# Optimization experiments

Hardware: AMD Instinct MI355X
Metric: run time of the kernel (lower is better)

Reference implementation:

```python
import jax, jax.numpy as jnp
import numpy as np

N, IN_DIM, HID, E_DIM, E = 50000, 128, 256, 32, 400000
BN_INV = np.float32(1.0 / np.sqrt(1.0 + 1e-5))  # running_mean=0, running_var=1


def _lin_init(key, fan_in, fan_out):
    kw, kb = jax.random.split(key)
    s = 1.0 / np.sqrt(fan_in)
    W = jax.random.uniform(kw, (fan_in, fan_out), jnp.float32, -s, s)
    b = jax.random.uniform(kb, (fan_out,), jnp.float32, -s, s)
    return W, b


def setup_inputs() -> dict:
    key = jax.random.key(0)
    ks = jax.random.split(key, 12)
    x = jax.random.normal(ks[0], (N, IN_DIM), jnp.float32)
    edge_index = jax.random.randint(ks[1], (2, E), 0, N, jnp.int64)
    edge_attr = jax.random.normal(ks[2], (E, E_DIM), jnp.float32)
    Wn, bn_b = _lin_init(ks[3], IN_DIM, HID)
    We, be = _lin_init(ks[4], E_DIM, HID)
    Wa1, ba1 = _lin_init(ks[5], 2 * HID, HID)
    Wa2, ba2 = _lin_init(ks[6], HID, 1)
    W1, b1 = _lin_init(ks[7], HID, 2 * HID)
    W2, b2 = _lin_init(ks[8], 2 * HID, HID)
    gn = jnp.ones((HID,), jnp.float32); betan = jnp.zeros((HID,), jnp.float32)
    ge = jnp.ones((HID,), jnp.float32); betae = jnp.zeros((HID,), jnp.float32)
    gm = jnp.ones((2 * HID,), jnp.float32); betam = jnp.zeros((2 * HID,), jnp.float32)
    eps = jnp.zeros((1,), jnp.float32)
    return dict(x=x, edge_index=edge_index, edge_attr=edge_attr,
                Wn=Wn, bn_b=bn_b, gn=gn, betan=betan,
                We=We, be=be, ge=ge, betae=betae,
                Wa1=Wa1, ba1=ba1, Wa2=Wa2, ba2=ba2,
                W1=W1, b1=b1, gm=gm, betam=betam, W2=W2, b2=b2, eps=eps)


def _bn(h, g, b):
    # eval-mode BatchNorm1d with running_mean=0, running_var=1
    return h * (g * BN_INV) + b


def reference(x, edge_index, edge_attr, Wn, bn_b, gn, betan, We, be, ge, betae,
              Wa1, ba1, Wa2, ba2, W1, b1, gm, betam, W2, b2, eps):
    h = jax.nn.relu(_bn(x @ Wn + bn_b, gn, betan))           # [N, HID] node_encoder
    ef = jax.nn.relu(_bn(edge_attr @ We + be, ge, betae))    # [E, HID] edge_encoder
    row, col = edge_index[0], edge_index[1]
    ni = h[row]                                              # [E, HID]
    nj = h[col]                                              # [E, HID]
    att_in = jnp.concatenate([ni + ef, nj], axis=-1)         # [E, 2*HID]
    a = jnp.tanh(att_in @ Wa1 + ba1) @ Wa2 + ba2             # [E, 1]
    a = jax.nn.leaky_relu(a, 0.2)
    a = jax.nn.softmax(a, axis=0)                            # softmax over all edges
    msg = (nj + ef) * a                                      # [E, HID]
    agg = jnp.zeros_like(h).at[row].add(msg)                 # scatter-add
    out = (1.0 + eps) * h + agg
    mid = jax.nn.relu(_bn(out @ W1 + b1, gm, betam))         # MLP hidden [N, 2*HID]
    return mid @ W2 + b2                                     # [N, HID]
```

## Files before the change

kernel.cpp:

```cpp
#include <hip/hip_runtime.h>

typedef __attribute__((ext_vector_type(8))) short    s16x8;
typedef __attribute__((ext_vector_type(8))) unsigned short u16x8;
typedef __attribute__((ext_vector_type(4))) unsigned short u16x4;
typedef __attribute__((ext_vector_type(4))) float    f32x4;

#define BN_INV 0.9999950000374997f
#define MAXDEG 64
#define INV64  0.015625f

__device__ __forceinline__ unsigned short f2b(float f) {
    union { float f; unsigned u; } v; v.f = f;
    return (unsigned short)((v.u + 0x7FFFu + ((v.u >> 16) & 1u)) >> 16);
}
__device__ __forceinline__ float b2f(unsigned short b) {
    union { unsigned u; float f; } v; v.u = (unsigned)b << 16;
    return v.f;
}
__device__ __forceinline__ float fast_tanh(float x) {
    float e = __expf(-2.f * fabsf(x));
    float t = (1.f - e) / (1.f + e);
    return copysignf(t, x);
}

__global__ __launch_bounds__(256) void gemm_mfma(
    const void* __restrict__ Av, int lda, int a_f32,
    const unsigned short* __restrict__ BT, int ldb, int bsplit,
    float* __restrict__ Cf, unsigned short* __restrict__ Cb, int ldc,
    const float* __restrict__ bias, const float* __restrict__ gamma,
    const float* __restrict__ beta, int M, int K, int bnrelu)
{
    __shared__ unsigned short As[128 * 40];
    __shared__ unsigned short Bs[128 * 40];

    const int tid = threadIdx.x;
    const int row0 = blockIdx.y * 128;
    const int col0 = blockIdx.x * 128;
    const int w = tid >> 6, l = tid & 63;
    const int wr = (w >> 1) * 64;
    const int wc = (w & 1) * 64;
    const int srow = tid >> 1;
    const int shalf = (tid & 1) * 16;

    f32x4 acc[4][4];
    #pragma unroll
    for (int i = 0; i < 4; ++i)
        #pragma unroll
        for (int j = 0; j < 4; ++j)
            acc[i][j] = (f32x4){0.f, 0.f, 0.f, 0.f};

    const bool arow_ok = (row0 + srow) < M;
    const unsigned short* Ab = (const unsigned short*)Av + (size_t)(row0 + srow) * lda + shalf;
    const float*          Af = (const float*)Av          + (size_t)(row0 + srow) * lda + shalf;
    int bcol = col0 + srow, koff = 0;
    if (bsplit && col0 >= bsplit) { bcol -= bsplit; koff = bsplit; }
    const unsigned short* Bp = BT + (size_t)bcol * ldb + koff + shalf;

    const int lrow = (l >> 4) * 4;
    const int lcol = l & 15;
    const int kfrag = (l >> 4) * 8;

    for (int kt = 0; kt < K; kt += 32) {
        u16x8 av0 = {0, 0, 0, 0, 0, 0, 0, 0};
        u16x8 av1 = {0, 0, 0, 0, 0, 0, 0, 0};
        if (arow_ok) {
            if (a_f32) {
                float4 u0 = *(const float4*)(Af + kt);
                float4 u1 = *(const float4*)(Af + kt + 4);
                float4 u2 = *(const float4*)(Af + kt + 8);
                float4 u3 = *(const float4*)(Af + kt + 12);
                av0 = (u16x8){ f2b(u0.x), f2b(u0.y), f2b(u0.z), f2b(u0.w),
                               f2b(u1.x), f2b(u1.y), f2b(u1.z), f2b(u1.w) };
                av1 = (u16x8){ f2b(u2.x), f2b(u2.y), f2b(u2.z), f2b(u2.w),
                               f2b(u3.x), f2b(u3.y), f2b(u3.z), f2b(u3.w) };
            } else {
                av0 = *(const u16x8*)(Ab + kt);
                av1 = *(const u16x8*)(Ab + kt + 8);
            }
        }
        u16x8 bv0 = *(const u16x8*)(Bp + kt);
        u16x8 bv1 = *(const u16x8*)(Bp + kt + 8);
        *(u16x8*)&As[srow * 40 + shalf]     = av0;
        *(u16x8*)&As[srow * 40 + shalf + 8] = av1;
        *(u16x8*)&Bs[srow * 40 + shalf]     = bv0;
        *(u16x8*)&Bs[srow * 40 + shalf + 8] = bv1;
        __syncthreads();
        s16x8 af[4], bfr[4];
        #pragma unroll
        for (int i = 0; i < 4; ++i)
            af[i] = *(const s16x8*)&As[(wr + i * 16 + lcol) * 40 + kfrag];
        #pragma unroll
        for (int j = 0; j < 4; ++j)
            bfr[j] = *(const s16x8*)&Bs[(wc + j * 16 + lcol) * 40 + kfrag];
        #pragma unroll
        for (int i = 0; i < 4; ++i)
            #pragma unroll
            for (int j = 0; j < 4; ++j)
                acc[i][j] = __builtin_amdgcn_mfma_f32_16x16x32_bf16(
                    af[i], bfr[j], acc[i][j], 0, 0, 0);
        __syncthreads();
    }

    #pragma unroll
    for (int j = 0; j < 4; ++j) {
        const int col = col0 + wc + j * 16 + lcol;
        const float bi = bias ? bias[col] : 0.f;
        float g = 1.f, bt = 0.f;
        if (bnrelu) { g = gamma[col] * BN_INV; bt = beta[col]; }
        #pragma unroll
        for (int i = 0; i < 4; ++i) {
            const int r0 = row0 + wr + i * 16 + lrow;
            #pragma unroll
            for (int q = 0; q < 4; ++q) {
                const int rr = r0 + q;
                if (rr < M) {
                    float v = acc[i][j][q] + bi;
                    if (bnrelu) v = fmaxf(v * g + bt, 0.f);
                    if (Cf) Cf[(size_t)rr * ldc + col] = v;
                    if (Cb) Cb[(size_t)rr * ldc + col] = f2b(v);
                }
            }
        }
    }
}

__global__ __launch_bounds__(512) void fused_edge(
    const float* __restrict__ ea,
    const int* __restrict__ ei,
    const unsigned short* __restrict__ WeT,
    const unsigned char* __restrict__ Wa1T8,
    const unsigned short* __restrict__ HAB,
    const float* __restrict__ be, const float* __restrict__ ge,
    const float* __restrict__ betae, const float* __restrict__ ba1,
    const float* __restrict__ Wa2, const float* __restrict__ ba2,
    unsigned char* __restrict__ EF,
    float* __restrict__ es, float* __restrict__ Ssum, int E)
{
    __shared__ __align__(16) unsigned char smem[32768];
    unsigned short* As  = (unsigned short*)smem;
    unsigned char*  EFs = smem;
    int*   sIdx = (int*)smem;
    float* sRed = (float*)(smem + 1024);

    const int tid = threadIdx.x;
    const int row0 = blockIdx.x * 128;
    const int w = tid >> 6, l = tid & 63;
    const int lgrp = l >> 4, lcol = l & 15;
    const int kfrag = lgrp * 8;

    {
        const int sr = tid >> 2, sk = (tid & 3) * 8;
        u16x8 av = {0, 0, 0, 0, 0, 0, 0, 0};
        if (row0 + sr < E) {
            const float* ap = ea + (size_t)(row0 + sr) * 32 + sk;
            float4 u0 = *(const float4*)ap, u1 = *(const float4*)(ap + 4);
            av = (u16x8){ f2b(u0.x), f2b(u0.y), f2b(u0.z), f2b(u0.w),
                          f2b(u1.x), f2b(u1.y), f2b(u1.z), f2b(u1.w) };
        }
        *(u16x8*)&As[sr * 40 + sk] = av;
    }
    __syncthreads();

    f32x4 acc[4][4];
    #pragma unroll
    for (int i = 0; i < 4; ++i)
        #pragma unroll
        for (int j = 0; j < 4; ++j)
            acc[i][j] = (f32x4){0.f, 0.f, 0.f, 0.f};

    const int wchan = (w & 3) * 64;
    const int wedge = (w >> 2) * 64;
    {
        s16x8 af[4], bfr[4];
        #pragma unroll
        for (int i = 0; i < 4; ++i)
            af[i] = *(const s16x8*)&WeT[(wchan + i * 16 + lcol) * 32 + kfrag];
        #pragma unroll
        for (int j = 0; j < 4; ++j)
            bfr[j] = *(const s16x8*)&As[(wedge + j * 16 + lcol) * 40 + kfrag];
        #pragma unroll
        for (int i = 0; i < 4; ++i)
            #pragma unroll
            for (int j = 0; j < 4; ++j)
                acc[i][j] = __builtin_amdgcn_mfma_f32_16x16x32_bf16(
                    af[i], bfr[j], acc[i][j], 0, 0, 0);
    }
    __syncthreads();

    #pragma unroll
    for (int i = 0; i < 4; ++i) {
        const int ch0 = wchan + i * 16 + lgrp * 4;
        float4 g4 = *(const float4*)(ge + ch0);
        float4 t4 = *(const float4*)(betae + ch0);
        float4 b4 = *(const float4*)(be + ch0);
        g4.x *= BN_INV; g4.y *= BN_INV; g4.z *= BN_INV; g4.w *= BN_INV;
        #pragma unroll
        for (int j = 0; j < 4; ++j) {
            const int edge = wedge + j * 16 + lcol;
            float v0 = fmaxf((acc[i][j][0] + b4.x) * g4.x + t4.x, 0.f);
            float v1 = fmaxf((acc[i][j][1] + b4.y) * g4.y + t4.y, 0.f);
            float v2 = fmaxf((acc[i][j][2] + b4.z) * g4.z + t4.z, 0.f);
            float v3 = fmaxf((acc[i][j][3] + b4.w) * g4.w + t4.w, 0.f);
            int pk = __builtin_amdgcn_cvt_pk_fp8_f32(v0, v1, 0, false);
            pk = __builtin_amdgcn_cvt_pk_fp8_f32(v2, v3, pk, true);
            *(unsigned*)&EFs[edge * 256 + ((((ch0 >> 3) ^ (edge & 7)) << 3) | (ch0 & 7))]
                = (unsigned)pk;
            acc[i][j] = (f32x4){0.f, 0.f, 0.f, 0.f};
        }
    }
    __syncthreads();

    const int wr = (w >> 2) * 64;
    const int wc = (w & 3) * 64;
    for (int kt = 0; kt < 256; kt += 32) {
        long af8[4], bf8[4];
        const int kb = (kt + kfrag) >> 3;
        #pragma unroll
        for (int i = 0; i < 4; ++i) {
            const int edge = wr + i * 16 + lcol;
            af8[i] = *(const long*)&EFs[edge * 256 + ((kb ^ (edge & 7)) << 3)];
        }
        #pragma unroll
        for (int j = 0; j < 4; ++j)
            bf8[j] = *(const long*)&Wa1T8[(size_t)(wc + j * 16 + lcol) * 256 + kt + kfrag];
        #pragma unroll
        for (int i = 0; i < 4; ++i)
            #pragma unroll
            for (int j = 0; j < 4; ++j)
                acc[i][j] = __builtin_amdgcn_mfma_f32_16x16x32_fp8_fp8(
                    af8[i], bf8[j], acc[i][j], 0, 0, 0);
    }

    {
        const int row = tid >> 2, cb = (tid & 3) * 64;
        if (row0 + row < E) {
            unsigned char* dst = EF + (size_t)(row0 + row) * 256 + cb;
            #pragma unroll
            for (int t2 = 0; t2 < 8; ++t2) {
                const int b = (cb >> 3) + t2;
                *(long*)(dst + t2 * 8)
                    = *(const long*)&EFs[row * 256 + ((b ^ (row & 7)) << 3)];
            }
        }
    }
    __syncthreads();

    if (tid < 128) {
        const int ge = row0 + tid;
        sIdx[tid]       = (ge < E) ? ei[ge] : 0;
        sIdx[128 + tid] = (ge < E) ? ei[E + ge] : 0;
    }
    __syncthreads();

    {
        int colv[4]; float ba1c[4], wa2c[4];
        #pragma unroll
        for (int j = 0; j < 4; ++j) {
            colv[j] = wc + j * 16 + lcol;
            ba1c[j] = ba1[colv[j]];
            wa2c[j] = Wa2[colv[j]];
        }
        #pragma unroll
        for (int i = 0; i < 4; ++i) {
            #pragma unroll
            for (int q = 0; q < 4; ++q) {
                const int row = wr + i * 16 + lgrp * 4 + q;
                const unsigned short* hap = HAB + (size_t)sIdx[row] * 512;
                const unsigned short* hbp = HAB + (size_t)sIdx[128 + row] * 512 + 256;
                float s = 0.f;
                #pragma unroll
                for (int j = 0; j < 4; ++j) {
                    float t = fast_tanh(acc[i][j][q] * INV64 + b2f(hap[colv[j]])
                                        + b2f(hbp[colv[j]]) + ba1c[j]);
                    s += t * wa2c[j];
                }
                s += __shfl_xor(s, 1); s += __shfl_xor(s, 2);
                s += __shfl_xor(s, 4); s += __shfl_xor(s, 8);
                if (lcol == 0) sRed[row * 4 + (w & 3)] = s;
            }
        }
    }
    __syncthreads();

    if (tid < 128) {
        const int ge = row0 + tid;
        float sv = sRed[tid * 4] + sRed[tid * 4 + 1]
                 + sRed[tid * 4 + 2] + sRed[tid * 4 + 3] + ba2[0];
        sv = sv > 0.f ? sv : 0.2f * sv;
        float ev = __expf(sv);
        float contrib = 0.f;
        if (ge < E) { es[ge] = ev; contrib = ev; }
        #pragma unroll
        for (int off = 32; off; off >>= 1) contrib += __shfl_xor(contrib, off);
        if (l == 0) atomicAdd(Ssum, contrib);
    }
}

__global__ __launch_bounds__(256) void fill_kernel(
    const int* __restrict__ ei, int* __restrict__ cnt, int* __restrict__ perm,
    int E)
{
    int e = blockIdx.x * 256 + threadIdx.x;
    const int stride = gridDim.x * 256;
    for (; e < E; e += stride) {
        const int r = ei[e];
        const int pos = atomicAdd(&cnt[r], 1);
        if (pos < MAXDEG) perm[(size_t)r * MAXDEG + pos] = e;
    }
}

__global__ __launch_bounds__(256) void gather_kernel(
    const int* __restrict__ ei, const unsigned char* __restrict__ EF,
    const unsigned short* __restrict__ h_bf, const float* __restrict__ es,
    const int* __restrict__ cnt, const int* __restrict__ perm,
    const float* __restrict__ eps, const float* __restrict__ Ssum,
    unsigned short* __restrict__ ob_bf, int N, int E)
{
    const int w = threadIdx.x >> 6, l = threadIdx.x & 63;
    const int r = blockIdx.x * 4 + w;
    if (r >= N) return;
    const int k0 = l * 4;

    const int deg = cnt[r] < MAXDEG ? cnt[r] : MAXDEG;
    const int pe = perm[(size_t)r * MAXDEG + l];
    const float esl = (l < deg) ? es[pe] : 0.f;
    const int   cl  = (l < deg) ? ei[E + pe] : 0;

    f32x4 acc = {0.f, 0.f, 0.f, 0.f};
    u16x4 hv_c = {0, 0, 0, 0}; int ef_c = 0; float es_c = 0.f;
    if (deg > 0) {
        const int e0 = __shfl(pe, 0), c0 = __shfl(cl, 0);
        es_c = __shfl(esl, 0);
        hv_c = *(const u16x4*)(h_bf + (size_t)c0 * 256 + k0);
        ef_c = *(const int*)(EF + (size_t)e0 * 256 + k0);
    }
    for (int p = 0; p < deg; ++p) {
        u16x4 hv_n = {0, 0, 0, 0}; int ef_n = 0; float es_n = 0.f;
        if (p + 1 < deg) {
            const int en = __shfl(pe, p + 1), cn = __shfl(cl, p + 1);
            es_n = __shfl(esl, p + 1);
            hv_n = *(const u16x4*)(h_bf + (size_t)cn * 256 + k0);
            ef_n = *(const int*)(EF + (size_t)en * 256 + k0);
        }
        acc[0] += es_c * (b2f(hv_c[0]) + __builtin_amdgcn_cvt_f32_fp8(ef_c, 0));
        acc[1] += es_c * (b2f(hv_c[1]) + __builtin_amdgcn_cvt_f32_fp8(ef_c, 1));
        acc[2] += es_c * (b2f(hv_c[2]) + __builtin_amdgcn_cvt_f32_fp8(ef_c, 2));
        acc[3] += es_c * (b2f(hv_c[3]) + __builtin_amdgcn_cvt_f32_fp8(ef_c, 3));
        hv_c = hv_n; ef_c = ef_n; es_c = es_n;
    }

    const float sc = 1.f + eps[0];
    const float invS = 1.f / Ssum[0];
    u16x4 hr = *(const u16x4*)(h_bf + (size_t)r * 256 + k0);
    u16x4 o = { f2b(sc * b2f(hr[0]) + acc[0] * invS),
                f2b(sc * b2f(hr[1]) + acc[1] * invS),
                f2b(sc * b2f(hr[2]) + acc[2] * invS),
                f2b(sc * b2f(hr[3]) + acc[3] * invS) };
    *(u16x4*)(ob_bf + (size_t)r * 256 + k0) = o;
}

__global__ __launch_bounds__(256) void prep_kernel(
    const float* __restrict__ Wn, const float* __restrict__ We,
    const float* __restrict__ Wa1, const float* __restrict__ W1,
    const float* __restrict__ W2,
    unsigned short* __restrict__ WnT, unsigned short* __restrict__ WeT,
    unsigned short* __restrict__ Wa1T, unsigned char* __restrict__ Wa1T8,
    unsigned short* __restrict__ W1T, unsigned short* __restrict__ W2T,
    int* __restrict__ cnt, float* __restrict__ Ssum, int N)
{
    const int b = blockIdx.x, t = threadIdx.x;
    { const int i = b * 256 + t; if (i < N) cnt[i] = 0; }
    if (b == 0 && t == 0) Ssum[0] = 0.f;
    if (b < 128) {
        WnT[t * 128 + b] = f2b(Wn[(size_t)b * 256 + t]);
    } else if (b < 160) {
        const int rr = b - 128;
        WeT[t * 32 + rr] = f2b(We[(size_t)rr * 256 + t]);
    } else if (b < 672) {
        const int rr = b - 160;
        const float v = Wa1[(size_t)rr * 256 + t];
        Wa1T[t * 512 + rr] = f2b(v);
        if (rr < 256) {
            int pk = __builtin_amdgcn_cvt_pk_fp8_f32(v * 64.f, 0.f, 0, false);
            Wa1T8[(size_t)t * 256 + rr] = (unsigned char)(pk & 0xFF);
        }
    } else if (b < 928) {
        const int rr = b - 672;
        W1T[(size_t)t * 256 + rr]         = f2b(W1[(size_t)rr * 512 + t]);
        W1T[(size_t)(t + 256) * 256 + rr] = f2b(W1[(size_t)rr * 512 + t + 256]);
    } else if (b < 1440) {
        const int rr = b - 928;
        W2T[(size_t)t * 512 + rr] = f2b(W2[(size_t)rr * 256 + t]);
    }
}

extern "C" void kernel_launch(void* const* d_in, const int* in_sizes, int n_in,
                              void* d_out, int out_size, void* d_ws, size_t ws_size,
                              hipStream_t stream)
{
    const float* x     = (const float*)d_in[0];
    const int*   ei    = (const int*)  d_in[1];
    const float* eattr = (const float*)d_in[2];
    const float* Wn    = (const float*)d_in[3];
    const float* bnb   = (const float*)d_in[4];
    const float* gn    = (const float*)d_in[5];
    const float* betan = (const float*)d_in[6];
    const float* We    = (const float*)d_in[7];
    const float* be    = (const float*)d_in[8];
    const float* ge    = (const float*)d_in[9];
    const float* betae = (const float*)d_in[10];
    const float* Wa1   = (const float*)d_in[11];
    const float* ba1   = (const float*)d_in[12];
    const float* Wa2   = (const float*)d_in[13];
    const float* ba2   = (const float*)d_in[14];
    const float* W1    = (const float*)d_in[15];
    const float* b1    = (const float*)d_in[16];
    const float* gm    = (const float*)d_in[17];
    const float* betam = (const float*)d_in[18];
    const float* W2    = (const float*)d_in[19];
    const float* b2    = (const float*)d_in[20];
    const float* eps   = (const float*)d_in[21];

    const int N = in_sizes[0] / 128;
    const int E = in_sizes[1] / 2;

    char* p = (char*)d_ws;
    auto alloc = [&](size_t bytes) {
        char* r = p; p += (bytes + 255) & ~(size_t)255; return r;
    };
    unsigned char*  EF    = (unsigned char*) alloc((size_t)E * 256);
    unsigned short* h_bf  = (unsigned short*)alloc((size_t)N * 256 * 2);
    unsigned short* HAB   = (unsigned short*)alloc((size_t)N * 512 * 2);
    float*          es    = (float*)         alloc((size_t)E * 4);
    int*            cnt   = (int*)            alloc((size_t)N * 4);
    int*            perm  = (int*)            alloc((size_t)N * MAXDEG * 4);
    float*          Ssum  = (float*)         alloc(256);
    unsigned short* WnT   = (unsigned short*)alloc(256 * 128 * 2);
    unsigned short* WeT   = (unsigned short*)alloc(256 * 32 * 2);
    unsigned short* Wa1T  = (unsigned short*)alloc(256 * 512 * 2);
    unsigned char*  Wa1T8 = (unsigned char*) alloc(256 * 256);
    unsigned short* W1T   = (unsigned short*)alloc(512 * 256 * 2);
    unsigned short* W2T   = (unsigned short*)alloc(256 * 512 * 2);
    unsigned short* ob_bf = HAB;
    unsigned short* mid   = (unsigned short*)EF;

    dim3 blk(256);
    const int rbN = (N + 127) / 128;

    prep_kernel<<<1440, blk, 0, stream>>>(Wn, We, Wa1, W1, W2,
        WnT, WeT, Wa1T, Wa1T8, W1T, W2T, cnt, Ssum, N);
    fill_kernel<<<512, blk, 0, stream>>>(ei, cnt, perm, E);

    gemm_mfma<<<dim3(2, rbN), blk, 0, stream>>>(x, 128, 1, WnT, 128, 0,
        nullptr, h_bf, 256, bnb, gn, betan, N, 128, 1);
    gemm_mfma<<<dim3(4, rbN), blk, 0, stream>>>(h_bf, 256, 0, Wa1T, 512, 256,
        nullptr, HAB, 512, nullptr, nullptr, nullptr, N, 256, 0);

    fused_edge<<<(E + 127) / 128, dim3(512), 0, stream>>>(
        eattr, ei, WeT, Wa1T8, HAB, be, ge, betae, ba1, Wa2, ba2,
        EF, es, Ssum, E);

    gather_kernel<<<(N + 3) / 4, blk, 0, stream>>>(ei, EF, h_bf, es,
        cnt, perm, eps, Ssum, ob_bf, N, E);

    gemm_mfma<<<dim3(4, rbN), blk, 0, stream>>>(ob_bf, 256, 0, W1T, 256, 0,
        nullptr, mid, 512, b1, gm, betam, N, 256, 1);
    gemm_mfma<<<dim3(2, rbN), blk, 0, stream>>>(mid, 512, 0, W2T, 512, 0,
        (float*)d_out, nullptr, 256, b2, nullptr, nullptr, N, 512, 0);
}
```

Before: 535.7 us.

## Shrink fused_edge to 64-edge blocks of 256 threads with separate index LDS

Restructures fused_edge so each block handles 64 edges with 4 waves, each wave owning a 64-channel slice, instead of 128 edges with 8 waves. LDS drops to about 18KB, and the edge-index loads move into the first staging phase in their own LDS region, which removes two barriers. The aim is more resident blocks per CU and less time lost at synchronisation. In exchange there are twice as many blocks, and the We and Wa1 weight fragments are reloaded per 64 edges instead of per 128.

```diff
diff --git a/kernel.cpp b/kernel.cpp
--- a/kernel.cpp
+++ b/kernel.cpp
@@ -124,7 +124,7 @@
     }
 }
 
-__global__ __launch_bounds__(512) void fused_edge(
+__global__ __launch_bounds__(256) void fused_edge(
     const float* __restrict__ ea,
     const int* __restrict__ ei,
     const unsigned short* __restrict__ WeT,
@@ -136,17 +136,18 @@
     unsigned char* __restrict__ EF,
     float* __restrict__ es, float* __restrict__ Ssum, int E)
 {
-    __shared__ __align__(16) unsigned char smem[32768];
+    __shared__ __align__(16) unsigned char smem[18432];
     unsigned short* As  = (unsigned short*)smem;
     unsigned char*  EFs = smem;
-    int*   sIdx = (int*)smem;
-    float* sRed = (float*)(smem + 1024);
+    int*   sIdx = (int*)(smem + 16384);
+    float* sRed = (float*)(smem + 16896);
 
     const int tid = threadIdx.x;
-    const int row0 = blockIdx.x * 128;
+    const int row0 = blockIdx.x * 64;
     const int w = tid >> 6, l = tid & 63;
     const int lgrp = l >> 4, lcol = l & 15;
     const int kfrag = lgrp * 8;
+    const int wc = w * 64;
 
     {
         const int sr = tid >> 2, sk = (tid & 3) * 8;
@@ -158,6 +159,8 @@
                           f2b(u1.x), f2b(u1.y), f2b(u1.z), f2b(u1.w) };
         }
         *(u16x8*)&As[sr * 40 + sk] = av;
+        if (tid < 64)       sIdx[tid] = (row0 + tid < E) ? ei[row0 + tid] : 0;
+        else if (tid < 128) sIdx[tid] = (row0 + tid - 64 < E) ? ei[E + row0 + tid - 64] : 0;
     }
     __syncthreads();
 
@@ -168,16 +171,14 @@
         for (int j = 0; j < 4; ++j)
             acc[i][j] = (f32x4){0.f, 0.f, 0.f, 0.f};
 
-    const int wchan = (w & 3) * 64;
-    const int wedge = (w >> 2) * 64;
     {
         s16x8 af[4], bfr[4];
         #pragma unroll
         for (int i = 0; i < 4; ++i)
-            af[i] = *(const s16x8*)&WeT[(wchan + i * 16 + lcol) * 32 + kfrag];
+            af[i] = *(const s16x8*)&WeT[(wc + i * 16 + lcol) * 32 + kfrag];
         #pragma unroll
         for (int j = 0; j < 4; ++j)
-            bfr[j] = *(const s16x8*)&As[(wedge + j * 16 + lcol) * 40 + kfrag];
+            bfr[j] = *(const s16x8*)&As[(j * 16 + lcol) * 40 + kfrag];
         #pragma unroll
         for (int i = 0; i < 4; ++i)
             #pragma unroll
@@ -189,14 +190,14 @@
 
     #pragma unroll
     for (int i = 0; i < 4; ++i) {
-        const int ch0 = wchan + i * 16 + lgrp * 4;
+        const int ch0 = wc + i * 16 + lgrp * 4;
         float4 g4 = *(const float4*)(ge + ch0);
         float4 t4 = *(const float4*)(betae + ch0);
         float4 b4 = *(const float4*)(be + ch0);
         g4.x *= BN_INV; g4.y *= BN_INV; g4.z *= BN_INV; g4.w *= BN_INV;
         #pragma unroll
         for (int j = 0; j < 4; ++j) {
-            const int edge = wedge + j * 16 + lcol;
+            const int edge = j * 16 + lcol;
             float v0 = fmaxf((acc[i][j][0] + b4.x) * g4.x + t4.x, 0.f);
             float v1 = fmaxf((acc[i][j][1] + b4.y) * g4.y + t4.y, 0.f);
             float v2 = fmaxf((acc[i][j][2] + b4.z) * g4.z + t4.z, 0.f);
@@ -210,14 +211,12 @@
     }
     __syncthreads();
 
-    const int wr = (w >> 2) * 64;
-    const int wc = (w & 3) * 64;
     for (int kt = 0; kt < 256; kt += 32) {
         long af8[4], bf8[4];
         const int kb = (kt + kfrag) >> 3;
         #pragma unroll
         for (int i = 0; i < 4; ++i) {
-            const int edge = wr + i * 16 + lcol;
+            const int edge = i * 16 + lcol;
             af8[i] = *(const long*)&EFs[edge * 256 + ((kb ^ (edge & 7)) << 3)];
         }
         #pragma unroll
@@ -243,14 +242,6 @@
             }
         }
     }
-    __syncthreads();
-
-    if (tid < 128) {
-        const int ge = row0 + tid;
-        sIdx[tid]       = (ge < E) ? ei[ge] : 0;
-        sIdx[128 + tid] = (ge < E) ? ei[E + ge] : 0;
-    }
-    __syncthreads();
 
     {
         int colv[4]; float ba1c[4], wa2c[4];
@@ -264,25 +255,25 @@
         for (int i = 0; i < 4; ++i) {
             #pragma unroll
             for (int q = 0; q < 4; ++q) {
-                const int row = wr + i * 16 + lgrp * 4 + q;
+                const int row = i * 16 + lgrp * 4 + q;
                 const unsigned short* hap = HAB + (size_t)sIdx[row] * 512;
-                const unsigned short* hbp = HAB + (size_t)sIdx[128 + row] * 512 + 256;
+                const unsigned short* hbp = HAB + (size_t)sIdx[64 + row] * 512 + 256;
                 float s = 0.f;
                 #pragma unroll
                 for (int j = 0; j < 4; ++j) {
-                    float t = fast_tanh(acc[i][j][q] * INV64 + b2f(hap[colv[j]])
-                                        + b2f(hbp[colv[j]]) + ba1c[j]);
+                    float t = fast_tanh(fmaf(acc[i][j][q], INV64,
+                                             b2f(hap[colv[j]]) + b2f(hbp[colv[j]]) + ba1c[j]));
                     s += t * wa2c[j];
                 }
                 s += __shfl_xor(s, 1); s += __shfl_xor(s, 2);
                 s += __shfl_xor(s, 4); s += __shfl_xor(s, 8);
-                if (lcol == 0) sRed[row * 4 + (w & 3)] = s;
+                if (lcol == 0) sRed[row * 4 + w] = s;
             }
         }
     }
     __syncthreads();
 
-    if (tid < 128) {
+    if (tid < 64) {
         const int ge = row0 + tid;
         float sv = sRed[tid * 4] + sRed[tid * 4 + 1]
                  + sRed[tid * 4 + 2] + sRed[tid * 4 + 3] + ba2[0];
@@ -456,7 +447,7 @@
     gemm_mfma<<<dim3(4, rbN), blk, 0, stream>>>(h_bf, 256, 0, Wa1T, 512, 256,
         nullptr, HAB, 512, nullptr, nullptr, nullptr, N, 256, 0);
 
-    fused_edge<<<(E + 127) / 128, dim3(512), 0, stream>>>(
+    fused_edge<<<(E + 63) / 64, blk, 0, stream>>>(
         eattr, ei, WeT, Wa1T8, HAB, be, ge, betae, ba1, Wa2, ba2,
         EF, es, Ssum, E);
 
```

New measurement: 534.5 us. Within noise of the previous version (-0.2%).
